# Kernel tuning notes

Hardware: AMD Instinct MI355X
Metric: run time of the kernel (lower is better)

## Reference

```python
import jax, jax.numpy as jnp
import numpy as np

SEQ = 8192
DIM = 1024

def setup_inputs() -> dict:
    key = jax.random.key(0)
    kx, kq, kk, kv1, kv2 = jax.random.split(key, 5)
    std = 0.01  # flax nn.initializers.normal() default stddev=1e-2
    return {
        "x": jax.random.normal(kx, (SEQ, DIM), dtype=jnp.float32),
        "wq": jax.random.normal(kq, (DIM, DIM), dtype=jnp.float32) * std,
        "wk": jax.random.normal(kk, (DIM, DIM), dtype=jnp.float32) * std,
        "wv1": jax.random.normal(kv1, (DIM, DIM), dtype=jnp.float32) * std,
        "wv2": jax.random.normal(kv2, (DIM, DIM), dtype=jnp.float32) * std,
    }

def reference(x, wq, wk, wv1, wv2):
    # x: [S, D]; single-head causal self-attention with SiLU-gated output proj
    q = x @ wq              # [S, D]
    k = x @ wk              # [S, D]
    v = x @ wv1             # [S, D]
    dim_head = q.shape[-1]
    dots = (q @ k.T) * (dim_head ** -0.5)          # [S, S]
    s = x.shape[-2]
    mask = jnp.tril(jnp.ones((s, s), dtype=bool))
    dots = jnp.where(mask, dots, -1e9)
    attn = jax.nn.softmax(dots, axis=-1)            # [S, S]
    hidden = attn @ v                               # [S, D]
    return jax.nn.silu(hidden) @ wv2                # [S, D]
```

## Files before the change

### kernel.cpp

```cpp
#include <hip/hip_runtime.h>
#include <hip/hip_bf16.h>
#include <cstdint>
#include <cstddef>

constexpr int SEQ = 8192;
constexpr int DIM = 1024;

typedef __attribute__((ext_vector_type(8))) short short8;
typedef __attribute__((ext_vector_type(4))) float f32x4;
typedef __attribute__((ext_vector_type(4))) unsigned short us4;

#define MFMA_BF16 __builtin_amdgcn_mfma_f32_16x16x32_bf16

static __device__ __forceinline__ unsigned short f2bf(float f) {
    uint32_t u = __builtin_bit_cast(uint32_t, f);
    u += 0x7FFFu + ((u >> 16) & 1u);
    return (unsigned short)(u >> 16);
}
static __device__ __forceinline__ float bf2f(unsigned short h) {
    uint32_t u = ((uint32_t)h) << 16;
    return __builtin_bit_cast(float, u);
}
static __device__ __forceinline__ int r64(int x) {
    return ((x + 32) >> 6) << 6;
}

#define GLOAD16(gp, lp) __builtin_amdgcn_global_load_lds(                      \
    (const __attribute__((address_space(1))) void*)(gp),                       \
    (__attribute__((address_space(3))) void*)(lp), 16, 0, 0)

template<int OM, bool CAUSAL, bool KCAP, bool SILU, bool SPLITK>
__global__ __launch_bounds__(256, 2)
void gemm_bt(const unsigned short* __restrict__ A,
             const unsigned short* __restrict__ Bt,
             void* __restrict__ Cp,
             int M, int N, int K, float scale, int rowBase, int NS)
{
    constexpr int BM = 128, BK = 64, BN = 128;
    constexpr int NF = BN / 32;
    __shared__ __align__(16) unsigned short As[2][BM * BK];
    __shared__ __align__(16) unsigned short Bs[2][BN * BK];

    const int t = threadIdx.x;
    const int lane = t & 63, w = t >> 6;
    const int wr = w >> 1, wc = w & 1;
    const int ln15 = lane & 15, hi = lane >> 4;

    const int gx = gridDim.x, gy = gridDim.y;
    const int nwg = gx * gy * gridDim.z;
    const int orig = blockIdx.y + gy * (blockIdx.x + gx * blockIdx.z);
    const int q = nwg >> 3, r8 = nwg & 7;
    const int xcd = orig & 7, idx = orig >> 3;
    const int wg = (xcd < r8 ? xcd * (q + 1)
                             : r8 * (q + 1) + (xcd - r8) * q) + idx;
    const int byi = wg % gy, tmpw = wg / gy;
    const int bxi = tmpw % gx, bzi = tmpw / gx;

    const int bm = byi * BM, bn = bxi * BN;

    if (CAUSAL && bn > rowBase + bm + (BM - 1)) return;
    int Keff = K;
    if (KCAP) { int kc = rowBase + bm + BM; Keff = kc < K ? kc : K; }
    int kbeg = 0, kend = Keff;
    if (SPLITK) {
        kbeg = r64(bzi * Keff / NS);
        int ke = r64((bzi + 1) * Keff / NS);
        kend = ke < Keff ? ke : Keff;
        if (kbeg >= kend) return;
    }

#define STAGE_TILES(buf, k0) do {                                              \
        _Pragma("unroll")                                                      \
        for (int i = 0; i < 4; ++i) {                                          \
            int c = t + 256 * i;                                               \
            int r = c >> 3, qq = (c & 7) ^ (r & 7);                            \
            GLOAD16(A + (size_t)(bm + r) * K + (k0) + qq * 8,                  \
                    &As[buf][c * 8]);                                          \
        }                                                                      \
        _Pragma("unroll")                                                      \
        for (int i = 0; i < 4; ++i) {                                          \
            int c = t + 256 * i;                                               \
            int r = c >> 3, qq = (c & 7) ^ (r & 7);                            \
            GLOAD16(Bt + (size_t)(bn + r) * K + (k0) + qq * 8,                 \
                    &Bs[buf][c * 8]);                                          \
        }                                                                      \
    } while (0)

    f32x4 acc[4][NF] = {};

    STAGE_TILES(0, kbeg);
    int cur = 0;
    for (int k0 = kbeg; k0 < kend; k0 += BK) {
        if (k0 + BK < kend) {
            STAGE_TILES(cur ^ 1, k0 + BK);
            asm volatile("s_waitcnt vmcnt(8)" ::: "memory");
        } else {
            asm volatile("s_waitcnt vmcnt(0)" ::: "memory");
        }
        __builtin_amdgcn_s_barrier();
        asm volatile("" ::: "memory");

        #pragma unroll
        for (int kk = 0; kk < 2; ++kk) {
            short8 a[4], b[NF];
            #pragma unroll
            for (int m = 0; m < 4; ++m) {
                int r = wr * 64 + m * 16 + ln15;
                int s = (kk * 4 + hi) ^ (r & 7);
                a[m] = *(const short8*)(&As[cur][r * 64 + s * 8]);
            }
            #pragma unroll
            for (int n = 0; n < NF; ++n) {
                int r = wc * 64 + n * 16 + ln15;
                int s = (kk * 4 + hi) ^ (r & 7);
                b[n] = *(const short8*)(&Bs[cur][r * 64 + s * 8]);
            }
            __builtin_amdgcn_s_setprio(1);
            #pragma unroll
            for (int m = 0; m < 4; ++m)
                #pragma unroll
                for (int n = 0; n < NF; ++n)
                    acc[m][n] = MFMA_BF16(a[m], b[n], acc[m][n], 0, 0, 0);
            __builtin_amdgcn_s_setprio(0);
        }
        asm volatile("" ::: "memory");
        __builtin_amdgcn_s_barrier();
        cur ^= 1;
    }
#undef STAGE_TILES

    float* Pz = (OM == 3)
        ? (float*)Cp + (size_t)bzi * M * N : nullptr;
    #pragma unroll
    for (int m = 0; m < 4; ++m)
        #pragma unroll
        for (int n = 0; n < NF; ++n)
            #pragma unroll
            for (int j = 0; j < 4; ++j) {
                int row = bm + wr * 64 + m * 16 + hi * 4 + j;
                int col = bn + wc * 64 + n * 16 + ln15;
                float v = acc[m][n][j] * scale;
                if (SILU) v = v / (1.0f + __expf(-v));
                if (OM == 0)
                    ((unsigned short*)Cp)[(size_t)row * N + col] = f2bf(v);
                else if (OM == 1)
                    ((unsigned short*)Cp)[(size_t)col * M + row] = f2bf(v);
                else if (OM == 2)
                    ((float*)Cp)[(size_t)row * N + col] = v;
                else
                    Pz[(size_t)row * N + col] = v;
            }
}

__global__ __launch_bounds__(256)
void reduce_silu(const float* __restrict__ part, unsigned short* __restrict__ out,
                 int ns, int rowBase)
{
    const size_t idx = ((size_t)blockIdx.x * 256 + threadIdx.x) * 8;
    const int r = (int)(idx >> 10);
    int keb = rowBase + ((r >> 7) << 7) + 128;
    if (keb > SEQ) keb = SEQ;

    f32x4 s0 = {}, s1 = {};
    for (int z = 0; z < ns; ++z) {
        int b0 = r64(z * keb / ns);
        int b1 = r64((z + 1) * keb / ns);
        if (b1 > keb) b1 = keb;
        if (b1 > b0) {
            const float* p = part + (size_t)z * (2048 * 1024) + idx;
            s0 += *(const f32x4*)p;
            s1 += *(const f32x4*)(p + 4);
        }
    }
    short8 o;
    #pragma unroll
    for (int j = 0; j < 4; ++j) {
        float v = s0[j];
        o[j] = (short)f2bf(v / (1.0f + __expf(-v)));
    }
    #pragma unroll
    for (int j = 0; j < 4; ++j) {
        float v = s1[j];
        o[4 + j] = (short)f2bf(v / (1.0f + __expf(-v)));
    }
    *(short8*)(out + idx) = o;
}

__global__ __launch_bounds__(256)
void softmax_rows(unsigned short* __restrict__ S, int rowBase)
{
    __shared__ float red[4];
    const int r = blockIdx.x;
    const int grow = rowBase + r;
    const int Kcap = ((grow >> 7) + 1) << 7;
    unsigned short* row = S + (size_t)r * SEQ;
    const int t = threadIdx.x, lane = t & 63, w = t >> 6;

    float v[4][8];
    float mx = -1e30f;
    #pragma unroll
    for (int i = 0; i < 4; ++i) {
        int c0 = (i * 256 + t) * 8;
        if (c0 < Kcap) {
            short8 s8 = *(const short8*)(row + c0);
            #pragma unroll
            for (int j = 0; j < 8; ++j) {
                float f = bf2f((unsigned short)s8[j]);
                v[i][j] = (c0 + j <= grow) ? f : -1e30f;
                mx = fmaxf(mx, v[i][j]);
            }
        } else {
            #pragma unroll
            for (int j = 0; j < 8; ++j) v[i][j] = -1e30f;
        }
    }
    #pragma unroll
    for (int off = 32; off >= 1; off >>= 1)
        mx = fmaxf(mx, __shfl_xor(mx, off, 64));
    if (lane == 0) red[w] = mx;
    __syncthreads();
    mx = fmaxf(fmaxf(red[0], red[1]), fmaxf(red[2], red[3]));
    __syncthreads();

    float sum = 0.f;
    #pragma unroll
    for (int i = 0; i < 4; ++i)
        #pragma unroll
        for (int j = 0; j < 8; ++j) {
            float p = (v[i][j] > -1e29f) ? __expf(v[i][j] - mx) : 0.f;
            v[i][j] = p;
            sum += p;
        }
    #pragma unroll
    for (int off = 32; off >= 1; off >>= 1)
        sum += __shfl_xor(sum, off, 64);
    if (lane == 0) red[w] = sum;
    __syncthreads();
    sum = red[0] + red[1] + red[2] + red[3];
    const float inv = 1.0f / sum;

    #pragma unroll
    for (int i = 0; i < 4; ++i) {
        int c0 = (i * 256 + t) * 8;
        if (c0 < Kcap) {
            short8 o;
            #pragma unroll
            for (int j = 0; j < 8; ++j) o[j] = (short)f2bf(v[i][j] * inv);
            *(short8*)(row + c0) = o;
        }
    }
}

__global__ __launch_bounds__(256)
void cvt_bf16(const float* __restrict__ X, unsigned short* __restrict__ Y)
{
    int i = (blockIdx.x * 256 + threadIdx.x) * 8;
    f32x4 v0 = *(const f32x4*)(X + i);
    f32x4 v1 = *(const f32x4*)(X + i + 4);
    short8 o = { (short)f2bf(v0[0]), (short)f2bf(v0[1]),
                 (short)f2bf(v0[2]), (short)f2bf(v0[3]),
                 (short)f2bf(v1[0]), (short)f2bf(v1[1]),
                 (short)f2bf(v1[2]), (short)f2bf(v1[3]) };
    *(short8*)(Y + i) = o;
}

__global__ __launch_bounds__(256)
void twT(const float* __restrict__ W, unsigned short* __restrict__ WT)
{
    __shared__ float tile[64][65];
    const int bx = blockIdx.x * 64, by = blockIdx.y * 64;
    const int t = threadIdx.x, rr = t >> 4, c4 = (t & 15) * 4;
    #pragma unroll
    for (int i = 0; i < 4; ++i) {
        int r = rr + i * 16;
        f32x4 v = *(const f32x4*)(W + (size_t)(by + r) * DIM + bx + c4);
        tile[r][c4 + 0] = v[0]; tile[r][c4 + 1] = v[1];
        tile[r][c4 + 2] = v[2]; tile[r][c4 + 3] = v[3];
    }
    __syncthreads();
    #pragma unroll
    for (int i = 0; i < 4; ++i) {
        int r = rr + i * 16;
        us4 o = { f2bf(tile[c4 + 0][r]), f2bf(tile[c4 + 1][r]),
                  f2bf(tile[c4 + 2][r]), f2bf(tile[c4 + 3][r]) };
        *(us4*)(WT + (size_t)(bx + r) * DIM + by + c4) = o;
    }
}

extern "C" void kernel_launch(void* const* d_in, const int* in_sizes, int n_in,
                              void* d_out, int out_size, void* d_ws, size_t ws_size,
                              hipStream_t stream)
{
    const float* x   = (const float*)d_in[0];
    const float* wq  = (const float*)d_in[1];
    const float* wk  = (const float*)d_in[2];
    const float* wv1 = (const float*)d_in[3];
    const float* wv2 = (const float*)d_in[4];

    const size_t BUF = (size_t)SEQ * DIM * sizeof(unsigned short);
    unsigned short* qbuf  = (unsigned short*)d_ws;
    unsigned short* kbuf  = qbuf + (size_t)SEQ * DIM;
    unsigned short* vtbuf = kbuf + (size_t)SEQ * DIM;
    float* part = (float*)((char*)d_ws + 3 * BUF);
    const size_t PSZ = (size_t)2048 * 1024 * sizeof(float);
    int nsplit = 0;
    if (ws_size >= 3 * BUF + 2 * PSZ) {
        size_t ns = (ws_size - 3 * BUF) / PSZ;
        nsplit = (int)(ns < 4 ? ns : 4);
    }

    unsigned short* xb    = (unsigned short*)d_out;
    unsigned short* wqT   = xb + (size_t)SEQ * DIM;
    unsigned short* wkT   = wqT + DIM * DIM;
    unsigned short* wv1T  = wkT + DIM * DIM;
    unsigned short* Sband = (unsigned short*)d_out;

    dim3 tg(16, 16);
    cvt_bf16<<<SEQ * DIM / 2048, 256, 0, stream>>>(x, xb);
    twT<<<tg, 256, 0, stream>>>(wq,  wqT);
    twT<<<tg, 256, 0, stream>>>(wk,  wkT);
    twT<<<tg, 256, 0, stream>>>(wv1, wv1T);

    dim3 gproj(DIM / 128, SEQ / 128);
    gemm_bt<0,false,false,false,false><<<gproj, 256, 0, stream>>>(
        xb, wqT,  qbuf,  SEQ, DIM, DIM, 1.0f, 0, 0);
    gemm_bt<0,false,false,false,false><<<gproj, 256, 0, stream>>>(
        xb, wkT,  kbuf,  SEQ, DIM, DIM, 1.0f, 0, 0);
    gemm_bt<1,false,false,false,false><<<gproj, 256, 0, stream>>>(
        xb, wv1T, vtbuf, SEQ, DIM, DIM, 1.0f, 0, 0);

    constexpr int BAND = 2048;
    for (int b = 0; b < 4; ++b) {
        const int rb = b * BAND;
        const int ncol = (rb + BAND) / 128;
        dim3 gq(ncol, BAND / 128);
        gemm_bt<0,true,false,false,false><<<gq, 256, 0, stream>>>(
            qbuf + (size_t)rb * DIM, kbuf, Sband, BAND, SEQ, DIM, 0.03125f, rb, 0);
        if (b == 3)
            twT<<<tg, 256, 0, stream>>>(wv2, kbuf);
        softmax_rows<<<BAND, 256, 0, stream>>>(Sband, rb);
        if (nsplit >= 2) {
            dim3 gpv(DIM / 128, BAND / 128, nsplit);
            gemm_bt<3,false,true,false,true><<<gpv, 256, 0, stream>>>(
                Sband, vtbuf, part, BAND, DIM, SEQ, 1.0f, rb, nsplit);
            reduce_silu<<<BAND * DIM / 2048, 256, 0, stream>>>(
                part, qbuf + (size_t)rb * DIM, nsplit, rb);
        } else {
            dim3 gpv(DIM / 128, BAND / 128);
            gemm_bt<0,false,true,true,false><<<gpv, 256, 0, stream>>>(
                Sband, vtbuf, qbuf + (size_t)rb * DIM, BAND, DIM, SEQ, 1.0f, rb, 0);
        }
    }

    gemm_bt<2,false,false,false,false><<<gproj, 256, 0, stream>>>(
        qbuf, kbuf, d_out, SEQ, DIM, DIM, 1.0f, 0, 0);
}
```

Measured before the change: 406.2 us.

## Drop LDS double buffering in favor of higher occupancy

Replaces the double-buffered LDS staging with a single buffer loaded synchronously each k-step and fenced by __syncthreads. The launch bound goes from 2 to 4 workgroups per CU, using the halved LDS footprint to run more waves that hide latency. In exchange, prefetch of the next tile no longer overlaps with MFMA work inside a block, and the 64 accumulator registers per thread must fit the tighter register budget, which may cause spills.

```diff
diff --git a/kernel.cpp b/kernel.cpp
--- a/kernel.cpp
+++ b/kernel.cpp
@@ -30,7 +30,7 @@
     (__attribute__((address_space(3))) void*)(lp), 16, 0, 0)
 
 template<int OM, bool CAUSAL, bool KCAP, bool SILU, bool SPLITK>
-__global__ __launch_bounds__(256, 2)
+__global__ __launch_bounds__(256, 4)
 void gemm_bt(const unsigned short* __restrict__ A,
              const unsigned short* __restrict__ Bt,
              void* __restrict__ Cp,
@@ -38,8 +38,8 @@
 {
     constexpr int BM = 128, BK = 64, BN = 128;
     constexpr int NF = BN / 32;
-    __shared__ __align__(16) unsigned short As[2][BM * BK];
-    __shared__ __align__(16) unsigned short Bs[2][BN * BK];
+    __shared__ __align__(16) unsigned short As[BM * BK];
+    __shared__ __align__(16) unsigned short Bs[BN * BK];
 
     const int t = threadIdx.x;
     const int lane = t & 63, w = t >> 6;
@@ -69,36 +69,22 @@
         if (kbeg >= kend) return;
     }
 
-#define STAGE_TILES(buf, k0) do {                                              \
-        _Pragma("unroll")                                                      \
-        for (int i = 0; i < 4; ++i) {                                          \
-            int c = t + 256 * i;                                               \
-            int r = c >> 3, qq = (c & 7) ^ (r & 7);                            \
-            GLOAD16(A + (size_t)(bm + r) * K + (k0) + qq * 8,                  \
-                    &As[buf][c * 8]);                                          \
-        }                                                                      \
-        _Pragma("unroll")                                                      \
-        for (int i = 0; i < 4; ++i) {                                          \
-            int c = t + 256 * i;                                               \
-            int r = c >> 3, qq = (c & 7) ^ (r & 7);                            \
-            GLOAD16(Bt + (size_t)(bn + r) * K + (k0) + qq * 8,                 \
-                    &Bs[buf][c * 8]);                                          \
-        }                                                                      \
-    } while (0)
-
     f32x4 acc[4][NF] = {};
 
-    STAGE_TILES(0, kbeg);
-    int cur = 0;
     for (int k0 = kbeg; k0 < kend; k0 += BK) {
-        if (k0 + BK < kend) {
-            STAGE_TILES(cur ^ 1, k0 + BK);
-            asm volatile("s_waitcnt vmcnt(8)" ::: "memory");
-        } else {
-            asm volatile("s_waitcnt vmcnt(0)" ::: "memory");
-        }
-        __builtin_amdgcn_s_barrier();
-        asm volatile("" ::: "memory");
+        #pragma unroll
+        for (int i = 0; i < 4; ++i) {
+            int c = t + 256 * i;
+            int r = c >> 3, qq = (c & 7) ^ (r & 7);
+            GLOAD16(A + (size_t)(bm + r) * K + k0 + qq * 8, As + c * 8);
+        }
+        #pragma unroll
+        for (int i = 0; i < 4; ++i) {
+            int c = t + 256 * i;
+            int r = c >> 3, qq = (c & 7) ^ (r & 7);
+            GLOAD16(Bt + (size_t)(bn + r) * K + k0 + qq * 8, Bs + c * 8);
+        }
+        __syncthreads();
 
         #pragma unroll
         for (int kk = 0; kk < 2; ++kk) {
@@ -107,13 +93,13 @@
             for (int m = 0; m < 4; ++m) {
                 int r = wr * 64 + m * 16 + ln15;
                 int s = (kk * 4 + hi) ^ (r & 7);
-                a[m] = *(const short8*)(&As[cur][r * 64 + s * 8]);
+                a[m] = *(const short8*)(As + r * 64 + s * 8);
             }
             #pragma unroll
             for (int n = 0; n < NF; ++n) {
                 int r = wc * 64 + n * 16 + ln15;
                 int s = (kk * 4 + hi) ^ (r & 7);
-                b[n] = *(const short8*)(&Bs[cur][r * 64 + s * 8]);
+                b[n] = *(const short8*)(Bs + r * 64 + s * 8);
             }
             __builtin_amdgcn_s_setprio(1);
             #pragma unroll
@@ -123,11 +109,8 @@
                     acc[m][n] = MFMA_BF16(a[m], b[n], acc[m][n], 0, 0, 0);
             __builtin_amdgcn_s_setprio(0);
         }
-        asm volatile("" ::: "memory");
-        __builtin_amdgcn_s_barrier();
-        cur ^= 1;
-    }
-#undef STAGE_TILES
+        __syncthreads();
+    }
 
     float* Pz = (OM == 3)
         ? (float*)Cp + (size_t)bzi * M * N : nullptr;
```

Result: faster. 387.4 us (-4.6%).
